# Kernel tuning notes

Hardware: AMD Instinct MI355X
Metric: run time of the kernel (lower is better)

The kernel has to match this reference:

```python
import math
import jax, jax.numpy as jnp
import numpy as np


def fht(x):
    """Normalized fast Hadamard transform over the last axis (size = power of 2)."""
    n = x.shape[-1]
    pre = x.shape[:-1]
    y = x.reshape(-1, n)
    h = 1
    while h < n:
        y = y.reshape(-1, n // (2 * h), 2, h)
        a = y[:, :, 0, :]
        b = y[:, :, 1, :]
        y = jnp.stack([a + b, a - b], axis=2)
        h *= 2
    return y.reshape(*pre, n) * jnp.float32(1.0 / math.sqrt(n))


def setup_inputs() -> dict:
    key = jax.random.key(0)
    ks = jax.random.split(key, 8)
    B, N, M, G = 8192, 4096, 4096, 512  # tokens, in_features(n_pad), out_features(m_pad), n_pad//8
    CB = 256  # E8 shell codebook entries (8-bit indices), each an 8-dim lattice point
    x = jax.random.normal(ks[0], (B, N), dtype=jnp.float32)
    Qidxs = jax.random.randint(ks[1], (M, G), 0, CB, dtype=jnp.int32)
    Qidxs2 = jax.random.randint(ks[2], (M, G), 0, CB, dtype=jnp.int32)
    SU = jax.random.rademacher(ks[3], (M,), dtype=jnp.float32)  # row sign vector
    SV = jax.random.rademacher(ks[4], (N,), dtype=jnp.float32)  # column sign vector
    codebook = jax.random.normal(ks[5], (CB, 8), dtype=jnp.float32)
    codebook2 = jax.random.normal(ks[6], (CB, 8), dtype=jnp.float32)
    Wscale = jnp.asarray(0.85, dtype=jnp.float32)
    inv_resid_scale = jnp.asarray(0.07, dtype=jnp.float32)  # nonzero -> stage-2 enabled
    return {"x": x, "Qidxs": Qidxs, "Qidxs2": Qidxs2, "SU": SU, "SV": SV,
            "codebook": codebook, "codebook2": codebook2,
            "Wscale": Wscale, "inv_resid_scale": inv_resid_scale}


def reference(x, Qidxs, Qidxs2, SU, SV, codebook, codebook2, Wscale, inv_resid_scale):
    # in_features == n_pad and out_features == m_pad here (powers of 2), so no pad/slice.
    m_pad, g = Qidxs.shape
    n_pad = g * 8
    # 1) input RHT: signs then Hadamard
    x_rht = fht(x * SV[None, :])  # (B, n_pad)
    # 2) dequantize weights in RHT domain: codebook lookup per 8-dim group + residual stage
    W_rht = codebook[Qidxs].reshape(m_pad, n_pad)
    W_rht = W_rht + codebook2[Qidxs2].reshape(m_pad, n_pad) * inv_resid_scale
    # 3) matmul in RHT domain with global scale
    y_rht = (x_rht @ W_rht.T) * Wscale  # (B, m_pad)
    # 4) output inverse RHT: Hadamard then signs
    y = fht(y_rht) * SU[None, :]
    return y
```

## Files before the change

### kernel.cpp

```cpp
#include <hip/hip_runtime.h>

#define B_DIM 8192
#define N_DIM 4096
#define M_DIM 4096
#define G_DIM 512

typedef short bf16x8 __attribute__((ext_vector_type(8)));
typedef float f32x4 __attribute__((ext_vector_type(4)));

typedef __attribute__((address_space(1))) const void gvoid_t;
typedef __attribute__((address_space(3))) void lvoid_t;

__device__ __forceinline__ void load_lds16(const void* g, void* l) {
    __builtin_amdgcn_global_load_lds((gvoid_t*)g, (lvoid_t*)l, 16, 0, 0);
}

__device__ __forceinline__ unsigned short f2bf(float f) {
    union { float f; unsigned int u; } v; v.f = f;
    unsigned int u = v.u;
    unsigned int r = (u + 0x7fffu + ((u >> 16) & 1u)) >> 16;
    return (unsigned short)r;
}
__device__ __forceinline__ float bf2f(unsigned short s) {
    union { unsigned int u; float f; } v; v.u = ((unsigned int)s) << 16;
    return v.f;
}

__device__ __forceinline__ void h16(float* v) {
#pragma unroll
    for (int h = 1; h < 16; h <<= 1) {
#pragma unroll
        for (int i = 0; i < 16; i++) {
            if (!(i & h)) {
                float a = v[i], b = v[i | h];
                v[i] = a + b;
                v[i | h] = a - b;
            }
        }
    }
}

__device__ __forceinline__ void h64(float* v) {
#pragma unroll
    for (int h = 1; h < 64; h <<= 1) {
#pragma unroll
        for (int i = 0; i < 64; i++) {
            if (!(i & h)) {
                float a = v[i], b = v[i | h];
                v[i] = a + b;
                v[i | h] = a - b;
            }
        }
    }
}

__global__ __launch_bounds__(256) void k_build_w(
    const int* __restrict__ q1, const int* __restrict__ q2,
    const float* __restrict__ cb1, const float* __restrict__ cb2,
    const float* __restrict__ wsp, const float* __restrict__ irsp,
    unsigned short* __restrict__ W) {
    __shared__ float c1[256 * 9];
    __shared__ float c2[256 * 9];
    int t = threadIdx.x;
#pragma unroll
    for (int j = 0; j < 8; j++) {
        c1[t * 9 + j] = cb1[t * 8 + j];
        c2[t * 9 + j] = cb2[t * 8 + j];
    }
    __syncthreads();
    float ws = wsp[0];
    float irs = irsp[0] * ws;
    int gid = blockIdx.x * 256 + t;
    int i1 = q1[gid] * 9;
    int i2 = q2[gid] * 9;
    union { unsigned short s[8]; int4 v; } o;
#pragma unroll
    for (int j = 0; j < 8; j++) {
        o.s[j] = f2bf(c1[i1 + j] * ws + c2[i2 + j] * irs);
    }
    *(int4*)(W + (size_t)gid * 8) = o.v;
}

__global__ __launch_bounds__(256) void k_hadw(
    unsigned short* __restrict__ W, int base_mul, int step, float scale) {
    int c = blockIdx.x * 256 + threadIdx.x;
    int base = blockIdx.y * base_mul;
    float v[64];
#pragma unroll
    for (int j = 0; j < 64; j++)
        v[j] = bf2f(W[(size_t)(base + j * step) * N_DIM + c]);
    h64(v);
#pragma unroll
    for (int j = 0; j < 64; j++)
        W[(size_t)(base + j * step) * N_DIM + c] = f2bf(v[j] * scale);
}

__global__ __launch_bounds__(64) void k_rht_in(
    const float* __restrict__ x, const float* __restrict__ SV,
    unsigned short* __restrict__ out) {
    __shared__ float lds[4352];
    int u = threadIdx.x;
    int row = blockIdx.x;
    const float* xr = x + (size_t)row * N_DIM;
    float v[4][16];
#pragma unroll
    for (int r = 0; r < 16; r++) {
        int n = 4 * u + (r << 8);
        float4 a = *(const float4*)(xr + n);
        float4 s = *(const float4*)(SV + n);
        v[0][r] = a.x * s.x * 0.015625f;
        v[1][r] = a.y * s.y * 0.015625f;
        v[2][r] = a.z * s.z * 0.015625f;
        v[3][r] = a.w * s.w * 0.015625f;
    }
#pragma unroll
    for (int i = 0; i < 4; i++) h16(v[i]);
#pragma unroll
    for (int r = 0; r < 16; r++) {
#pragma unroll
        for (int i = 0; i < 4; i++) {
            int n = (r << 8) + 4 * u + i;
            lds[n + (n >> 4)] = v[i][r];
        }
    }
    __syncthreads();
#pragma unroll
    for (int j = 0; j < 4; j++) {
        int base = 17 * (u + (j << 6));
        float w[16];
#pragma unroll
        for (int n0 = 0; n0 < 16; n0++) w[n0] = lds[base + n0];
        h16(w);
#pragma unroll
        for (int n0 = 0; n0 < 16; n0++) lds[base + n0] = w[n0];
    }
    __syncthreads();
#pragma unroll
    for (int j = 0; j < 4; j++) {
        int base = 272 * ((u >> 4) + (j << 2)) + (u & 15);
        float w[16];
#pragma unroll
        for (int r = 0; r < 16; r++) w[r] = lds[base + 17 * r];
        h16(w);
#pragma unroll
        for (int r = 0; r < 16; r++) lds[base + 17 * r] = w[r];
    }
    __syncthreads();
    unsigned short* orow = out + (size_t)row * N_DIM;
#pragma unroll
    for (int s = 0; s < 8; s++) {
        int n = 8 * u + (s << 9);
        union { unsigned short h[8]; int4 q; } o;
#pragma unroll
        for (int jj = 0; jj < 8; jj++) {
            int nn = n + jj;
            o.h[jj] = f2bf(lds[nn + (nn >> 4)]);
        }
        *(int4*)(orow + n) = o.q;
    }
}

__global__ __launch_bounds__(512, 2) void k_gemm(
    const unsigned short* __restrict__ A,
    const unsigned short* __restrict__ Bw,
    const float* __restrict__ SU,
    float* __restrict__ C) {
    __shared__ __align__(16) unsigned short lds[4 * 16384];

    int t = threadIdx.x;
    int w = t >> 6;
    int l = t & 63;

    int lin = blockIdx.x;
    int xcd = lin & 7;
    int idx = lin >> 3;
    int bn = xcd * 2 + (idx >> 5);
    int bm = idx & 31;

    int lx = l ^ (l >> 3);
    const unsigned short* aS0 =
        A + (size_t)(bm * 256 + w * 16 + (lx >> 2)) * N_DIM + (lx & 3) * 8;
    const unsigned short* aS1 = aS0 + (size_t)128 * N_DIM;
    const unsigned short* bS0 =
        Bw + (size_t)(bn * 256 + w * 16 + (lx >> 2)) * N_DIM + (lx & 3) * 8;
    const unsigned short* bS1 = bS0 + (size_t)128 * N_DIM;

    int wm = w >> 2;
    int wn = w & 3;
    int quad = l >> 4;
    int ln = l & 15;
    unsigned aOff =
        (unsigned)((((wm * 128 + ln) << 6) | (quad << 4)) ^ ((ln >> 1) << 4)) >> 1;
    unsigned bOff = 8192u +
        ((unsigned)((((wn * 64 + ln) << 6) | (quad << 4)) ^ ((ln >> 1) << 4)) >> 1);

    f32x4 acc[8][4];
#pragma unroll
    for (int i = 0; i < 8; i++)
#pragma unroll
        for (int j = 0; j < 4; j++) {
            f32x4 z = {0.f, 0.f, 0.f, 0.f};
            acc[i][j] = z;
        }

#define STAGE(KT) do {                                              \
        int kt_ = (KT);                                             \
        int ks_ = kt_ < 127 ? kt_ : 127;                            \
        unsigned short* d_ = lds + ((unsigned)kt_ & 3u) * 16384 + w * 512; \
        load_lds16(aS0 + ks_ * 32, d_);                             \
        load_lds16(aS1 + ks_ * 32, d_ + 4096);                      \
        load_lds16(bS0 + ks_ * 32, d_ + 8192);                      \
        load_lds16(bS1 + ks_ * 32, d_ + 12288);                     \
    } while (0)

    STAGE(0);
    STAGE(1);
    STAGE(2);
    asm volatile("s_waitcnt vmcnt(8)");
    __builtin_amdgcn_s_barrier();
    asm volatile("" ::: "memory");

    for (int k = 0; k < N_DIM / 32; k++) {
        STAGE(k + 3);

        const unsigned short* aP = lds + ((unsigned)k & 3u) * 16384u + aOff;
        const unsigned short* bP = lds + ((unsigned)k & 3u) * 16384u + bOff;
        bf16x8 af[8], bfr[4];
#pragma unroll
        for (int j = 0; j < 4; j++) bfr[j] = *(const bf16x8*)(bP + j * 512);
#pragma unroll
        for (int i = 0; i < 8; i++) af[i] = *(const bf16x8*)(aP + i * 512);
#pragma unroll
        for (int i = 0; i < 8; i++)
#pragma unroll
            for (int j = 0; j < 4; j++)
                acc[i][j] = __builtin_amdgcn_mfma_f32_16x16x32_bf16(
                    af[i], bfr[j], acc[i][j], 0, 0, 0);

        asm volatile("s_waitcnt lgkmcnt(0)" ::: "memory");
        asm volatile("s_waitcnt vmcnt(8)");
        __builtin_amdgcn_s_barrier();
        asm volatile("" ::: "memory");
    }
    asm volatile("s_waitcnt vmcnt(0)");

#pragma unroll
    for (int j = 0; j < 4; j++) {
        int col = bn * 256 + wn * 64 + j * 16 + ln;
        float su = SU[col];
#pragma unroll
        for (int i = 0; i < 8; i++) {
#pragma unroll
            for (int r = 0; r < 4; r++) {
                int rowg = bm * 256 + wm * 128 + i * 16 + quad * 4 + r;
                C[(size_t)rowg * M_DIM + col] = acc[i][j][r] * su;
            }
        }
    }
#undef STAGE
}

extern "C" void kernel_launch(void* const* d_in, const int* in_sizes, int n_in,
                              void* d_out, int out_size, void* d_ws, size_t ws_size,
                              hipStream_t stream) {
    const float* x    = (const float*)d_in[0];
    const int*   q1   = (const int*)d_in[1];
    const int*   q2   = (const int*)d_in[2];
    const float* SU   = (const float*)d_in[3];
    const float* SV   = (const float*)d_in[4];
    const float* cb1  = (const float*)d_in[5];
    const float* cb2  = (const float*)d_in[6];
    const float* wsp  = (const float*)d_in[7];
    const float* irsp = (const float*)d_in[8];
    float* out = (float*)d_out;

    unsigned short* xrht = (unsigned short*)d_ws;
    unsigned short* Wb   = xrht + (size_t)B_DIM * N_DIM;

    k_build_w<<<dim3((M_DIM * G_DIM) / 256), dim3(256), 0, stream>>>(
        q1, q2, cb1, cb2, wsp, irsp, Wb);
    k_hadw<<<dim3(N_DIM / 256, 64), dim3(256), 0, stream>>>(Wb, 1, 64, 1.0f);
    k_hadw<<<dim3(N_DIM / 256, 64), dim3(256), 0, stream>>>(Wb, 64, 1, 0.015625f);
    k_rht_in<<<dim3(B_DIM), dim3(64), 0, stream>>>(x, SV, xrht);
    k_gemm<<<dim3(512), dim3(512), 0, stream>>>(xrht, Wb, SU, out);
}
```

Measured before the change: 534.2 us.

## Load B fragments directly from global into registers, halve LDS staging

The weight (B) operand is no longer staged through LDS. Each wave loads its B fragments straight from global memory into double-buffered registers one k-step ahead, while A keeps its 4-deep LDS pipeline in half the LDS. Block-to-tile mapping also changes so consecutive blocks on an XCD alternate bn and walk bm, which changes L2 reuse patterns. The aim is to cut LDS traffic and footprint. The cost is uncoalesced 16-byte strided global loads for B and duplicated B loads across waves sharing wn, and the vmcnt accounting becomes fragile.

```diff
diff --git a/kernel.cpp b/kernel.cpp
--- a/kernel.cpp
+++ b/kernel.cpp
@@ -165,7 +165,7 @@
     const unsigned short* __restrict__ Bw,
     const float* __restrict__ SU,
     float* __restrict__ C) {
-    __shared__ __align__(16) unsigned short lds[4 * 16384];
+    __shared__ __align__(16) unsigned short lds[4 * 8192];
 
     int t = threadIdx.x;
     int w = t >> 6;
@@ -174,16 +174,13 @@
     int lin = blockIdx.x;
     int xcd = lin & 7;
     int idx = lin >> 3;
-    int bn = xcd * 2 + (idx >> 5);
-    int bm = idx & 31;
+    int bn = xcd * 2 + (idx & 1);
+    int bm = idx >> 1;
 
     int lx = l ^ (l >> 3);
     const unsigned short* aS0 =
         A + (size_t)(bm * 256 + w * 16 + (lx >> 2)) * N_DIM + (lx & 3) * 8;
     const unsigned short* aS1 = aS0 + (size_t)128 * N_DIM;
-    const unsigned short* bS0 =
-        Bw + (size_t)(bn * 256 + w * 16 + (lx >> 2)) * N_DIM + (lx & 3) * 8;
-    const unsigned short* bS1 = bS0 + (size_t)128 * N_DIM;
 
     int wm = w >> 2;
     int wn = w & 3;
@@ -191,8 +188,10 @@
     int ln = l & 15;
     unsigned aOff =
         (unsigned)((((wm * 128 + ln) << 6) | (quad << 4)) ^ ((ln >> 1) << 4)) >> 1;
-    unsigned bOff = 8192u +
-        ((unsigned)((((wn * 64 + ln) << 6) | (quad << 4)) ^ ((ln >> 1) << 4)) >> 1);
+    const unsigned short* bp[4];
+#pragma unroll
+    for (int j = 0; j < 4; j++)
+        bp[j] = Bw + (size_t)(bn * 256 + wn * 64 + j * 16 + ln) * N_DIM + quad * 8;
 
     f32x4 acc[8][4];
 #pragma unroll
@@ -203,44 +202,54 @@
             acc[i][j] = z;
         }
 
-#define STAGE(KT) do {                                              \
+#define STAGE_A(KT) do {                                            \
         int kt_ = (KT);                                             \
         int ks_ = kt_ < 127 ? kt_ : 127;                            \
-        unsigned short* d_ = lds + ((unsigned)kt_ & 3u) * 16384 + w * 512; \
+        unsigned short* d_ = lds + ((unsigned)kt_ & 3u) * 8192 + w * 512; \
         load_lds16(aS0 + ks_ * 32, d_);                             \
         load_lds16(aS1 + ks_ * 32, d_ + 4096);                      \
-        load_lds16(bS0 + ks_ * 32, d_ + 8192);                      \
-        load_lds16(bS1 + ks_ * 32, d_ + 12288);                     \
     } while (0)
 
-    STAGE(0);
-    STAGE(1);
-    STAGE(2);
-    asm volatile("s_waitcnt vmcnt(8)");
+#define LOADB(DST, KT) do {                                         \
+        int kb_ = (KT) < 127 ? (KT) : 127;                          \
+        _Pragma("unroll")                                           \
+        for (int j = 0; j < 4; j++)                                 \
+            DST[j] = *(const bf16x8*)(bp[j] + kb_ * 32);            \
+    } while (0)
+
+    bf16x8 bA[4], bB[4];
+    LOADB(bA, 0);
+    STAGE_A(0);
+    STAGE_A(1);
+    STAGE_A(2);
+    asm volatile("s_waitcnt vmcnt(4)");
     __builtin_amdgcn_s_barrier();
     asm volatile("" ::: "memory");
 
-    for (int k = 0; k < N_DIM / 32; k++) {
-        STAGE(k + 3);
-
-        const unsigned short* aP = lds + ((unsigned)k & 3u) * 16384u + aOff;
-        const unsigned short* bP = lds + ((unsigned)k & 3u) * 16384u + bOff;
-        bf16x8 af[8], bfr[4];
-#pragma unroll
-        for (int j = 0; j < 4; j++) bfr[j] = *(const bf16x8*)(bP + j * 512);
-#pragma unroll
-        for (int i = 0; i < 8; i++) af[i] = *(const bf16x8*)(aP + i * 512);
-#pragma unroll
-        for (int i = 0; i < 8; i++)
-#pragma unroll
-            for (int j = 0; j < 4; j++)
-                acc[i][j] = __builtin_amdgcn_mfma_f32_16x16x32_bf16(
-                    af[i], bfr[j], acc[i][j], 0, 0, 0);
-
-        asm volatile("s_waitcnt lgkmcnt(0)" ::: "memory");
-        asm volatile("s_waitcnt vmcnt(8)");
-        __builtin_amdgcn_s_barrier();
-        asm volatile("" ::: "memory");
+#define BODY(K, BCUR, BNXT) do {                                    \
+        STAGE_A((K) + 3);                                           \
+        LOADB(BNXT, (K) + 1);                                       \
+        const unsigned short* aP =                                  \
+            lds + ((unsigned)(K) & 3u) * 8192u + aOff;              \
+        bf16x8 af[8];                                               \
+        _Pragma("unroll")                                           \
+        for (int i = 0; i < 8; i++) af[i] = *(const bf16x8*)(aP + i * 512); \
+        _Pragma("unroll")                                           \
+        for (int i = 0; i < 8; i++)                                 \
+            _Pragma("unroll")                                       \
+            for (int j = 0; j < 4; j++)                             \
+                acc[i][j] = __builtin_amdgcn_mfma_f32_16x16x32_bf16( \
+                    af[i], BCUR[j], acc[i][j], 0, 0, 0);            \
+        asm volatile("s_waitcnt lgkmcnt(0)");                       \
+        asm volatile("s_waitcnt vmcnt(6)");                         \
+        asm volatile("" ::: "memory");                              \
+        __builtin_amdgcn_s_barrier();                               \
+        asm volatile("" ::: "memory");                              \
+    } while (0)
+
+    for (int k = 0; k < N_DIM / 32; k += 2) {
+        BODY(k, bA, bB);
+        BODY(k + 1, bB, bA);
     }
     asm volatile("s_waitcnt vmcnt(0)");
 
@@ -257,7 +266,9 @@
             }
         }
     }
-#undef STAGE
+#undef STAGE_A
+#undef LOADB
+#undef BODY
 }
 
 extern "C" void kernel_launch(void* const* d_in, const int* in_sizes, int n_in,
```

Measured after the change: 628.7 us. 1.18x slower.
